# Kernel tuning notes

Hardware: AMD Instinct MI355X
Metric: run time of the kernel (lower is better)

Reference implementation:

```python
import jax, jax.numpy as jnp
import numpy as np

D_MODEL = 1024
N_HEADS = 16
D_HEAD = D_MODEL // N_HEADS


def setup_inputs() -> dict:
    key = jax.random.key(0)
    k1, k2, k3 = jax.random.split(key, 3)
    x = jax.random.normal(k1, (4, 2048, D_MODEL), dtype=jnp.float32)
    # nn.Linear weights stored [out, in]; we keep that convention.
    s = 1.0 / np.sqrt(D_MODEL)
    W_qkv = jax.random.uniform(k2, (3 * D_MODEL, D_MODEL), dtype=jnp.float32, minval=-s, maxval=s)
    W_out = jax.random.uniform(k3, (D_MODEL, D_MODEL), dtype=jnp.float32, minval=-s, maxval=s)
    return {"x": x, "W_qkv": W_qkv, "W_out": W_out}


def reference(x, W_qkv, W_out):
    B, T, C = x.shape
    qkv = jnp.einsum('btc,oc->bto', x, W_qkv)  # [B,T,3C]
    q, k, v = jnp.split(qkv, 3, axis=-1)

    def split_heads(t):
        return t.reshape(B, T, N_HEADS, D_HEAD).transpose(0, 2, 1, 3)  # [B,H,T,Dh]

    q, k, v = split_heads(q), split_heads(k), split_heads(v)
    scale = D_HEAD ** -0.5
    scores = jnp.einsum('bhqd,bhkd->bhqk', q, k) * scale  # [B,H,T,T]
    mask = jnp.triu(jnp.ones((T, T), dtype=bool), k=1)
    scores = jnp.where(mask, -jnp.inf, scores)
    att = jax.nn.softmax(scores, axis=-1)
    out = jnp.einsum('bhqk,bhkd->bhqd', att, v)
    out = out.transpose(0, 2, 1, 3).reshape(B, T, C)
    return jnp.einsum('btc,oc->bto', out, W_out)
```

## Files before the change

### kernel.cpp

```cpp
#include <hip/hip_runtime.h>
#include <hip/hip_bf16.h>
#include <math.h>


typedef __attribute__((ext_vector_type(8))) short bf16x8;
typedef __attribute__((ext_vector_type(4))) float f32x4;

__device__ __forceinline__ void async16(const void* g, void* l) {
    __builtin_amdgcn_global_load_lds((const __attribute__((address_space(1))) void*)g,
                                     (__attribute__((address_space(3))) void*)l,
                                     16, 0, 0);
}

__device__ __forceinline__ unsigned short f2b(float f) {
    __hip_bfloat16 h = __float2bfloat16(f);
    return *(unsigned short*)&h;
}

__device__ __forceinline__ unsigned int packbf2(float a, float b) {
    __hip_bfloat162 h2 = __float22bfloat162_rn(make_float2(a, b));
    return *(unsigned int*)&h2;
}

__global__ __launch_bounds__(256)
void cast3_f32_bf16(const float* __restrict__ a, unsigned short* __restrict__ oa, int na,
                    const float* __restrict__ b, unsigned short* __restrict__ ob, int nb,
                    const float* __restrict__ c, unsigned short* __restrict__ oc, int nc)
{
    const int bid  = blockIdx.x;
    const int na_b = na >> 11;
    const int nb_b = nb >> 11;
    const float* in;
    unsigned short* out;
    int base;
    if (bid < na_b)             { in = a; out = oa; base = bid; }
    else if (bid < na_b + nb_b) { in = b; out = ob; base = bid - na_b; }
    else                        { in = c; out = oc; base = bid - na_b - nb_b; }
    int i = (base * 256 + threadIdx.x) * 8;
    float4 x = *(const float4*)(in + i);
    float4 y = *(const float4*)(in + i + 4);
    __hip_bfloat16 r[8];
    r[0] = __float2bfloat16(x.x); r[1] = __float2bfloat16(x.y);
    r[2] = __float2bfloat16(x.z); r[3] = __float2bfloat16(x.w);
    r[4] = __float2bfloat16(y.x); r[5] = __float2bfloat16(y.y);
    r[6] = __float2bfloat16(y.z); r[7] = __float2bfloat16(y.w);
    *(float4*)(out + i) = *(float4*)r;
}

template <typename OutT>
__global__ __launch_bounds__(256)
void gemm_bf16_nt(const unsigned short* __restrict__ A,
                  const unsigned short* __restrict__ Bt,
                  OutT* __restrict__ C, int M, int N, int K,
                  int sc_ncols, float sc)
{
    __shared__ unsigned short As[2 * 128 * 32];
    __shared__ unsigned short Bs[2 * 128 * 32];
    const int tid  = threadIdx.x;
    const int lane = tid & 63;
    const int wave = tid >> 6;
    const int wm   = wave >> 1;
    const int wn   = wave & 1;
    const int m0   = blockIdx.y * 128;
    const int n0   = blockIdx.x * 128;

    f32x4 acc[4][4];
#pragma unroll
    for (int i = 0; i < 4; ++i)
#pragma unroll
        for (int j = 0; j < 4; ++j) acc[i][j] = (f32x4){0.f, 0.f, 0.f, 0.f};

    const int srow = tid >> 2;
    const int scol = (tid & 3) * 8;
    const int wbase = wave * 512;
    const int fr = lane & 15;
    const int fk = (lane >> 4) * 8;

    for (int k0 = 0; k0 < K; k0 += 64) {
#pragma unroll
        for (int ks = 0; ks < 2; ++ks) {
#pragma unroll
            for (int c = 0; c < 2; ++c) {
                const unsigned short* ga =
                    A + (size_t)(m0 + c * 64 + srow) * K + k0 + ks * 32 + scol;
                async16(ga, As + ks * 4096 + c * 2048 + wbase);
                const unsigned short* gb =
                    Bt + (size_t)(n0 + c * 64 + srow) * K + k0 + ks * 32 + scol;
                async16(gb, Bs + ks * 4096 + c * 2048 + wbase);
            }
        }
        __syncthreads();

#pragma unroll
        for (int ks = 0; ks < 2; ++ks) {
            bf16x8 af[4], bfr[4];
#pragma unroll
            for (int mi = 0; mi < 4; ++mi)
                af[mi] = *(const bf16x8*)&As[ks * 4096 + (wm * 64 + mi * 16 + fr) * 32 + fk];
#pragma unroll
            for (int ni = 0; ni < 4; ++ni)
                bfr[ni] = *(const bf16x8*)&Bs[ks * 4096 + (wn * 64 + ni * 16 + fr) * 32 + fk];
#pragma unroll
            for (int mi = 0; mi < 4; ++mi)
#pragma unroll
                for (int ni = 0; ni < 4; ++ni)
                    acc[mi][ni] = __builtin_amdgcn_mfma_f32_16x16x32_bf16(
                        af[mi], bfr[ni], acc[mi][ni], 0, 0, 0);
        }
        __syncthreads();
    }

    const int ccol  = n0 + wn * 64 + (lane & 15);
    const int crow0 = m0 + wm * 64 + (lane >> 4) * 4;
#pragma unroll
    for (int mi = 0; mi < 4; ++mi) {
#pragma unroll
        for (int r = 0; r < 4; ++r) {
            const size_t row = (size_t)(crow0 + mi * 16 + r);
#pragma unroll
            for (int ni = 0; ni < 4; ++ni) {
                float mult = (ccol + ni * 16 < sc_ncols) ? sc : 1.0f;
                float v = acc[mi][ni][r] * mult;
                if constexpr (__is_same(OutT, float)) {
                    C[row * N + ccol + ni * 16] = v;
                } else {
                    C[row * N + ccol + ni * 16] = f2b(v);
                }
            }
        }
    }
}

__global__ __launch_bounds__(256)
void transpose_v(const unsigned short* __restrict__ qkv, unsigned short* __restrict__ vt, int T)
{
    __shared__ unsigned short tile[64 * 72];
    const int tid = threadIdx.x;
    const int k0  = blockIdx.x * 64;
    const int h   = blockIdx.y;
    const int b   = blockIdx.z;
    const size_t C3 = 3072;
    const unsigned short* vb = qkv + (size_t)b * T * C3 + 2048 + h * 64;

    const int r  = tid >> 2;
    const int c0 = (tid & 3) * 16;
    {
        const unsigned short* g = vb + (size_t)(k0 + r) * C3 + c0;
        *(float4*)&tile[r * 72 + c0]     = *(const float4*)g;
        *(float4*)&tile[r * 72 + c0 + 8] = *(const float4*)(g + 8);
    }
    __syncthreads();
    unsigned short buf[16];
#pragma unroll
    for (int j = 0; j < 16; ++j) buf[j] = tile[(c0 + j) * 72 + r];
    unsigned short* o = vt + ((size_t)(b * 16 + h) * 64 + r) * T + k0 + c0;
    *(float4*)o       = *(float4*)&buf[0];
    *(float4*)(o + 8) = *(float4*)&buf[8];
}

__global__ __launch_bounds__(256, 4)
void attn_mfma(const unsigned short* __restrict__ qkv,
               const unsigned short* __restrict__ vt,
               unsigned short* __restrict__ out, int T)
{
    __shared__ unsigned short Ks[64 * 72];
    __shared__ unsigned short Vts[64 * 72];
    __shared__ unsigned short Ps[2][64 * 72];

    const int tid  = threadIdx.x;
    const int lane = tid & 63;
    const int wave = tid >> 6;
    const int lc   = lane & 15;
    const int quad = lane >> 4;
    const int nq   = T >> 6;
    const int bid  = blockIdx.x;
    const int bh   = bid & 63;
    const int a    = bid >> 6;
    const int b    = bh >> 4;
    const int h    = bh & 15;
    int qt[2];
    qt[0] = nq - 1 - a;
    qt[1] = a;
    const size_t C3 = 3072;
    const unsigned short* qb  = qkv + (size_t)b * T * C3 + h * 64;
    const unsigned short* kb  = qb + 1024;
    const unsigned short* vtb = vt + (size_t)(b * 16 + h) * 64 * T;

    const int sr = tid >> 2;
    const int sc = (tid & 3) * 16;

    const int qrow = wave * 16 + lc;
    bf16x8 qf[2][2];
#pragma unroll
    for (int t = 0; t < 2; ++t) {
        const unsigned short* gq = qb + (size_t)(qt[t] * 64 + qrow) * C3 + quad * 8;
        qf[t][0] = *(const bf16x8*)gq;
        qf[t][1] = *(const bf16x8*)(gq + 32);
    }

    f32x4 o_[2][4];
    float l_[2];
#pragma unroll
    for (int t = 0; t < 2; ++t) {
        l_[t] = 0.f;
#pragma unroll
        for (int i = 0; i < 4; ++i) o_[t][i] = (f32x4){0.f, 0.f, 0.f, 0.f};
    }

    const float MB = 8.0f;

    for (int kt = 0; kt <= qt[0]; ++kt) {
        const int k0 = kt * 64;
        const unsigned short* gk = kb + (size_t)(k0 + sr) * C3 + sc;
        float4 kv0 = *(const float4*)gk;
        float4 kv1 = *(const float4*)(gk + 8);
        const unsigned short* gv = vtb + (size_t)sr * T + k0 + sc;
        float4 vv0 = *(const float4*)gv;
        float4 vv1 = *(const float4*)(gv + 8);

        __syncthreads();
        *(float4*)&Ks[sr * 72 + sc]      = kv0;
        *(float4*)&Ks[sr * 72 + sc + 8]  = kv1;
        *(float4*)&Vts[sr * 72 + sc]     = vv0;
        *(float4*)&Vts[sr * 72 + sc + 8] = vv1;
        __syncthreads();

        bf16x8 ak[4][2];
#pragma unroll
        for (int mi = 0; mi < 4; ++mi) {
            ak[mi][0] = *(const bf16x8*)&Ks[(mi * 16 + lc) * 72 + quad * 8];
            ak[mi][1] = *(const bf16x8*)&Ks[(mi * 16 + lc) * 72 + 32 + quad * 8];
        }

#pragma unroll
        for (int t = 0; t < 2; ++t) {
            if (t == 1 && kt > qt[1]) break;
            f32x4 s[4];
#pragma unroll
            for (int mi = 0; mi < 4; ++mi) {
                s[mi] = (f32x4){0.f, 0.f, 0.f, 0.f};
                s[mi] = __builtin_amdgcn_mfma_f32_16x16x32_bf16(ak[mi][0], qf[t][0], s[mi], 0, 0, 0);
                s[mi] = __builtin_amdgcn_mfma_f32_16x16x32_bf16(ak[mi][1], qf[t][1], s[mi], 0, 0, 0);
            }
            if (kt == qt[t]) {
                const int qg = qt[t] * 64 + wave * 16 + lc;
                const int kbase = k0 + quad * 4;
#pragma unroll
                for (int mi = 0; mi < 4; ++mi)
#pragma unroll
                    for (int r = 0; r < 4; ++r)
                        if (kbase + mi * 16 + r > qg)
                            s[mi][r] = -__builtin_inff();
            }
            float lacc = 0.f;
            const int prow = (wave * 16 + lc) * 72 + quad * 4;
#pragma unroll
            for (int mi = 0; mi < 4; ++mi) {
                float p0 = __builtin_amdgcn_exp2f(s[mi][0] - MB);
                float p1 = __builtin_amdgcn_exp2f(s[mi][1] - MB);
                float p2 = __builtin_amdgcn_exp2f(s[mi][2] - MB);
                float p3 = __builtin_amdgcn_exp2f(s[mi][3] - MB);
                lacc += (p0 + p1) + (p2 + p3);
                uint2 pk;
                pk.x = packbf2(p0, p1);
                pk.y = packbf2(p2, p3);
                *(uint2*)&Ps[t][prow + mi * 16] = pk;
            }
            l_[t] += lacc;
        }

        bf16x8 av[4][2];
#pragma unroll
        for (int mi = 0; mi < 4; ++mi) {
            av[mi][0] = *(const bf16x8*)&Vts[(mi * 16 + lc) * 72 + quad * 8];
            av[mi][1] = *(const bf16x8*)&Vts[(mi * 16 + lc) * 72 + 32 + quad * 8];
        }

#pragma unroll
        for (int t = 0; t < 2; ++t) {
            if (t == 1 && kt > qt[1]) break;
            bf16x8 bp0 = *(const bf16x8*)&Ps[t][(wave * 16 + lc) * 72 + quad * 8];
            bf16x8 bp1 = *(const bf16x8*)&Ps[t][(wave * 16 + lc) * 72 + 32 + quad * 8];
#pragma unroll
            for (int mi = 0; mi < 4; ++mi) {
                o_[t][mi] = __builtin_amdgcn_mfma_f32_16x16x32_bf16(av[mi][0], bp0, o_[t][mi], 0, 0, 0);
                o_[t][mi] = __builtin_amdgcn_mfma_f32_16x16x32_bf16(av[mi][1], bp1, o_[t][mi], 0, 0, 0);
            }
        }
    }

#pragma unroll
    for (int t = 0; t < 2; ++t) {
        float rs = l_[t];
        rs += __shfl_xor(rs, 16);
        rs += __shfl_xor(rs, 32);
        float inv = 1.f / rs;
        unsigned short* ob = out + ((size_t)b * T + qt[t] * 64 + wave * 16 + lc) * 1024
                           + h * 64 + quad * 4;
#pragma unroll
        for (int mi = 0; mi < 4; ++mi) {
            uint2 pk;
            pk.x = packbf2(o_[t][mi][0] * inv, o_[t][mi][1] * inv);
            pk.y = packbf2(o_[t][mi][2] * inv, o_[t][mi][3] * inv);
            *(uint2*)(ob + mi * 16) = pk;
        }
    }
}

extern "C" void kernel_launch(void* const* d_in, const int* in_sizes, int n_in,
                              void* d_out, int out_size, void* d_ws, size_t ws_size,
                              hipStream_t stream)
{
    const float* x     = (const float*)d_in[0];
    const float* W_qkv = (const float*)d_in[1];
    const float* W_out = (const float*)d_in[2];
    float* out = (float*)d_out;

    const int C = 1024;
    const int T = 2048;
    const int M = in_sizes[0] / C;
    const int B = M / T;
    const int n_x    = in_sizes[0];
    const int n_wqkv = in_sizes[1];
    const int n_wout = in_sizes[2];

    unsigned short* x_bf    = (unsigned short*)d_ws;
    unsigned short* wqkv_bf = x_bf    + n_x;
    unsigned short* wout_bf = wqkv_bf + n_wqkv;
    unsigned short* qkv_bf  = wout_bf + n_wout;
    unsigned short* vt_bf   = qkv_bf  + (size_t)M * 3 * C;
    unsigned short* ao_bf   = vt_bf   + (size_t)B * 16 * 64 * T;

    cast3_f32_bf16<<<(n_x + n_wqkv + n_wout) / 2048, 256, 0, stream>>>(
        x, x_bf, n_x, W_qkv, wqkv_bf, n_wqkv, W_out, wout_bf, n_wout);

    const float QSC = 0.18033688011112042f;
    gemm_bf16_nt<unsigned short><<<dim3((3*C)/128, M/128), 256, 0, stream>>>(
        x_bf, wqkv_bf, qkv_bf, M, 3*C, C, C, QSC);

    transpose_v<<<dim3(T/64, 16, B), 256, 0, stream>>>(qkv_bf, vt_bf, T);

    const int nq = T / 64;
    attn_mfma<<<dim3(B * 16 * (nq / 2)), 256, 0, stream>>>(qkv_bf, vt_bf, ao_bf, T);

    gemm_bf16_nt<float><<<dim3(C/128, M/128), 256, 0, stream>>>(
        ao_bf, wout_bf, out, M, C, C, 0, 1.0f);
}
```

Measured before the change: 249.7 us.

## Replace QKV projection GEMM with 256x256 eight-phase pipelined MFMA kernel

Adds a new bf16 NT GEMM for the QKV projection. It uses 512 threads, 256x256 output tiles with a 64-wide K step, double-buffered async global-to-LDS loads with an XOR swizzle, and an explicit eight-phase schedule. That schedule interleaves LDS reads, MFMA bursts at raised priority and staged prefetches, separated by barriers and pinned waitcnts. The block index is also remapped across XCD groups to improve L2 locality. The aim is better MFMA utilisation and less global and LDS stall time than the old 128x128 kernel. The cost is heavy register and LDS pressure (128KB of LDS per block) and many barriers per iteration.

Result: no change. 250.7 us (+0.4%).

```diff
diff --git a/kernel.cpp b/kernel.cpp
--- a/kernel.cpp
+++ b/kernel.cpp
@@ -47,6 +47,161 @@
     *(float4*)(out + i) = *(float4*)r;
 }
 
+#define BAR8 __builtin_amdgcn_s_barrier()
+#define LGKM0_PIN do { asm volatile("s_waitcnt lgkmcnt(0)" ::: "memory"); \
+                       __builtin_amdgcn_sched_barrier(0); } while (0)
+#define VMCNT_PIN(n) do { asm volatile("s_waitcnt vmcnt(" #n ")" ::: "memory"); \
+                          __builtin_amdgcn_sched_barrier(0); } while (0)
+
+#define LOAD_A_ALL(B_) do { \
+    _Pragma("unroll") \
+    for (int mi = 0; mi < 8; ++mi) { \
+        af[mi][0] = *(const bf16x8*)&smem[(B_)*16384 + baseA0 + mi*1024]; \
+        af[mi][1] = *(const bf16x8*)&smem[(B_)*16384 + baseA1 + mi*1024]; \
+    } } while (0)
+
+#define LOAD_B2(B_, QN) do { \
+    _Pragma("unroll") \
+    for (int ni = 0; ni < 2; ++ni) { \
+        bf[ni][0] = *(const bf16x8*)&smem[(B_)*16384 + baseB0 + ((QN)*2+ni)*1024]; \
+        bf[ni][1] = *(const bf16x8*)&smem[(B_)*16384 + baseB1 + ((QN)*2+ni)*1024]; \
+    } } while (0)
+
+#define MFMA16(QM, QN) do { \
+    _Pragma("unroll") \
+    for (int mi = 0; mi < 4; ++mi) { \
+        _Pragma("unroll") \
+        for (int ni = 0; ni < 2; ++ni) { \
+            acc[(QM)*4+mi][(QN)*2+ni] = __builtin_amdgcn_mfma_f32_16x16x32_bf16( \
+                af[(QM)*4+mi][0], bf[ni][0], acc[(QM)*4+mi][(QN)*2+ni], 0, 0, 0); \
+            acc[(QM)*4+mi][(QN)*2+ni] = __builtin_amdgcn_mfma_f32_16x16x32_bf16( \
+                af[(QM)*4+mi][1], bf[ni][1], acc[(QM)*4+mi][(QN)*2+ni], 0, 0, 0); \
+        } } } while (0)
+
+#define STAGE_A8(B_, H_, T_) do { \
+    const unsigned short* g_ = A + (size_t)(m0 + (H_)*128) * K + (T_)*64; \
+    async16(g_ + g0, &smem[(B_)*16384 + (H_)*8192 + lds0]); \
+    async16(g_ + g1, &smem[(B_)*16384 + (H_)*8192 + lds1]); } while (0)
+
+#define STAGE_B8(B_, H_, T_) do { \
+    const unsigned short* g_ = Bt + (size_t)(n0 + (H_)*128) * K + (T_)*64; \
+    async16(g_ + g0, &smem[32768 + (B_)*16384 + (H_)*8192 + lds0]); \
+    async16(g_ + g1, &smem[32768 + (B_)*16384 + (H_)*8192 + lds1]); } while (0)
+
+__global__ __launch_bounds__(512, 2)
+void gemm_bf16_nt_8ph(const unsigned short* __restrict__ A,
+                      const unsigned short* __restrict__ Bt,
+                      unsigned short* __restrict__ C,
+                      int M, int N, int K, int sc_ncols, float sc)
+{
+    __shared__ unsigned short smem[65536];
+
+    const int tid  = threadIdx.x;
+    const int lane = tid & 63;
+    const int wave = tid >> 6;
+    const int wm   = wave >> 2;
+    const int wn   = wave & 3;
+    const int fr   = lane & 15;
+    const int q    = lane >> 4;
+
+    const int ntn = N >> 8;
+    int wg = blockIdx.x;
+    const int nwg = gridDim.x;
+    if ((nwg & 7) == 0) {
+        const int cpx = nwg >> 3;
+        wg = (wg & 7) * cpx + (wg >> 3);
+    }
+    const int m0 = (wg / ntn) << 8;
+    const int n0 = (wg % ntn) << 8;
+
+    const int c0 = tid, c1 = 512 + tid;
+    const int r0 = c0 >> 3, r1 = c1 >> 3;
+    const int g0 = r0 * K + (((c0 & 7) ^ (r0 & 7)) << 3);
+    const int g1 = r1 * K + (((c1 & 7) ^ (r1 & 7)) << 3);
+    const int lds0 = wave * 512;
+    const int lds1 = 4096 + wave * 512;
+
+    const int baseA0 = (wm*128 + fr) * 64 + (((0) | q) ^ (fr & 7)) * 8;
+    const int baseA1 = (wm*128 + fr) * 64 + (((4) | q) ^ (fr & 7)) * 8;
+    const int baseB0 = 32768 + (wn*64 + fr) * 64 + (((0) | q) ^ (fr & 7)) * 8;
+    const int baseB1 = 32768 + (wn*64 + fr) * 64 + (((4) | q) ^ (fr & 7)) * 8;
+
+    f32x4 acc[8][4];
+#pragma unroll
+    for (int i = 0; i < 8; ++i)
+#pragma unroll
+        for (int j = 0; j < 4; ++j) acc[i][j] = (f32x4){0.f, 0.f, 0.f, 0.f};
+
+    bf16x8 af[8][2];
+    bf16x8 bf[2][2];
+
+    STAGE_A8(0, 0, 0); STAGE_A8(0, 1, 0); STAGE_B8(0, 0, 0); STAGE_B8(0, 1, 0);
+    STAGE_A8(1, 0, 1); STAGE_A8(1, 1, 1); STAGE_B8(1, 0, 1);
+    VMCNT_PIN(6);
+    BAR8;
+
+    const int niter = K >> 7;
+#pragma unroll 1
+    for (int i = 0; i < niter; ++i) {
+        const int t1 = 2*i + 1, t2 = 2*i + 2, t3 = 2*i + 3;
+        const bool st = (i < niter - 1);
+
+        LOAD_A_ALL(0); LOAD_B2(0, 0);
+        STAGE_B8(1, 1, t1);
+        BAR8; LGKM0_PIN;
+        __builtin_amdgcn_s_setprio(1); MFMA16(0, 0); __builtin_amdgcn_s_setprio(0);
+        BAR8;
+        if (st) STAGE_A8(0, 0, t2);
+        BAR8; LGKM0_PIN;
+        __builtin_amdgcn_s_setprio(1); MFMA16(1, 0); __builtin_amdgcn_s_setprio(0);
+        BAR8;
+        LOAD_B2(0, 1);
+        if (st) STAGE_A8(0, 1, t2);
+        BAR8; LGKM0_PIN;
+        __builtin_amdgcn_s_setprio(1); MFMA16(0, 1); __builtin_amdgcn_s_setprio(0);
+        BAR8;
+        if (st) STAGE_B8(0, 0, t2);
+        BAR8; LGKM0_PIN;
+        __builtin_amdgcn_s_setprio(1); MFMA16(1, 1); __builtin_amdgcn_s_setprio(0);
+        if (st) { VMCNT_PIN(6); } else { VMCNT_PIN(0); }
+        BAR8;
+        LOAD_A_ALL(1); LOAD_B2(1, 0);
+        if (st) STAGE_B8(0, 1, t2);
+        BAR8; LGKM0_PIN;
+        __builtin_amdgcn_s_setprio(1); MFMA16(0, 0); __builtin_amdgcn_s_setprio(0);
+        BAR8;
+        if (st) STAGE_A8(1, 0, t3);
+        BAR8; LGKM0_PIN;
+        __builtin_amdgcn_s_setprio(1); MFMA16(1, 0); __builtin_amdgcn_s_setprio(0);
+        BAR8;
+        LOAD_B2(1, 1);
+        if (st) STAGE_A8(1, 1, t3);
+        BAR8; LGKM0_PIN;
+        __builtin_amdgcn_s_setprio(1); MFMA16(0, 1); __builtin_amdgcn_s_setprio(0);
+        BAR8;
+        if (st) STAGE_B8(1, 0, t3);
+        BAR8; LGKM0_PIN;
+        __builtin_amdgcn_s_setprio(1); MFMA16(1, 1); __builtin_amdgcn_s_setprio(0);
+        if (st) VMCNT_PIN(6);
+        BAR8;
+    }
+
+    const int ccol  = n0 + wn * 64 + fr;
+    const int crow0 = m0 + wm * 128 + q * 4;
+#pragma unroll
+    for (int mi = 0; mi < 8; ++mi) {
+#pragma unroll
+        for (int r = 0; r < 4; ++r) {
+            const size_t row = (size_t)(crow0 + mi * 16 + r);
+#pragma unroll
+            for (int ni = 0; ni < 4; ++ni) {
+                float mult = (ccol + ni * 16 < sc_ncols) ? sc : 1.0f;
+                C[row * N + ccol + ni * 16] = f2b(acc[mi][ni][r] * mult);
+            }
+        }
+    }
+}
+
 template <typename OutT>
 __global__ __launch_bounds__(256)
 void gemm_bf16_nt(const unsigned short* __restrict__ A,
@@ -335,7 +490,7 @@
         x, x_bf, n_x, W_qkv, wqkv_bf, n_wqkv, W_out, wout_bf, n_wout);
 
     const float QSC = 0.18033688011112042f;
-    gemm_bf16_nt<unsigned short><<<dim3((3*C)/128, M/128), 256, 0, stream>>>(
+    gemm_bf16_nt_8ph<<<dim3(((3*C) / 256) * (M / 256)), 512, 0, stream>>>(
         x_bf, wqkv_bf, qkv_bf, M, 3*C, C, C, QSC);
 
     transpose_v<<<dim3(T/64, 16, B), 256, 0, stream>>>(qkv_bf, vt_bf, T);
```
